# Kernel tuning notes

Measured on AMD Instinct MI355X. Metric: run time of the kernel, lower is better.

## Reference

```python
import jax, jax.numpy as jnp
import numpy as np

B, S, D = 4, 1024, 1024
H = 16
DK = D // H  # 64
F = 4096
EPS = 1e-6


def layer_norm(x, gamma, beta):
    mu = jnp.mean(x, axis=-1, keepdims=True)
    var = jnp.mean(jnp.square(x - mu), axis=-1, keepdims=True)
    return (x - mu) * jax.lax.rsqrt(var + EPS) * gamma + beta


def setup_inputs() -> dict:
    key = jax.random.key(0)
    ks = jax.random.split(key, 16)
    sd = 0.02
    return {
        "x": jax.random.normal(ks[0], (B, S, D), dtype=jnp.float32),
        "Wq": jax.random.normal(ks[1], (H, D, DK), dtype=jnp.float32) * sd,
        "bq": jnp.zeros((H, DK), dtype=jnp.float32),
        "Wk": jax.random.normal(ks[2], (H, D, DK), dtype=jnp.float32) * sd,
        "bk": jnp.zeros((H, DK), dtype=jnp.float32),
        "Wv": jax.random.normal(ks[3], (H, D, DK), dtype=jnp.float32) * sd,
        "bv": jnp.zeros((H, DK), dtype=jnp.float32),
        "Wo": jax.random.normal(ks[4], (D, D), dtype=jnp.float32) * sd,
        "bo": jnp.zeros((D,), dtype=jnp.float32),
        "W1": jax.random.normal(ks[5], (D, F), dtype=jnp.float32) * sd,
        "b1": jnp.zeros((F,), dtype=jnp.float32),
        "W2": jax.random.normal(ks[6], (F, D), dtype=jnp.float32) * sd,
        "b2": jnp.zeros((D,), dtype=jnp.float32),
        "g1": jnp.ones((D,), dtype=jnp.float32),
        "be1": jnp.zeros((D,), dtype=jnp.float32),
        "g2": jnp.ones((D,), dtype=jnp.float32),
        "be2": jnp.zeros((D,), dtype=jnp.float32),
    }


def reference(x, Wq, bq, Wk, bk, Wv, bv, Wo, bo, W1, b1, W2, b2, g1, be1, g2, be2):
    # Per-head Dense projections, expressed as one batched einsum.
    # q/k/v: [B, H, S, DK]
    q = jnp.einsum('bsd,hdk->bhsk', x, Wq) + bq[:, None, :]
    k = jnp.einsum('bsd,hdk->bhsk', x, Wk) + bk[:, None, :]
    v = jnp.einsum('bsd,hdk->bhsk', x, Wv) + bv[:, None, :]
    scale = 1.0 / jnp.sqrt(jnp.float32(DK))
    scores = jnp.einsum('bhqk,bhsk->bhqs', q, k) * scale  # [B,H,S,S]
    attn = jax.nn.softmax(scores, axis=-1)
    ctx = jnp.einsum('bhqs,bhsk->bhqk', attn, v)  # [B,H,S,DK]
    # concat heads along last dim -> [B,S,D]
    ctx = jnp.transpose(ctx, (0, 2, 1, 3)).reshape(B, S, D)
    mh = ctx @ Wo + bo
    # dropout is identity at inference
    h1 = layer_norm(mh + x, g1, be1)
    ffn = jax.nn.relu(h1 @ W1 + b1) @ W2 + b2
    out = layer_norm(h1 + ffn, g2, be2)
    return out
```

## Files before the change

### kernel.cpp

```cpp
#include <hip/hip_runtime.h>
#include <hip/hip_bf16.h>
#include <stdint.h>


typedef __bf16 bf16x8 __attribute__((ext_vector_type(8)));
typedef __bf16 bf16x4 __attribute__((ext_vector_type(4)));
typedef float f32x4 __attribute__((ext_vector_type(4)));

__device__ __forceinline__ f32x4 mfma16(bf16x8 a, bf16x8 b, f32x4 c) {
  return __builtin_amdgcn_mfma_f32_16x16x32_bf16(a, b, c, 0, 0, 0);
}

__device__ __forceinline__ void gload_lds16(const void* g, void* l) {
  typedef const unsigned int __attribute__((address_space(1)))* GP;
  typedef unsigned int __attribute__((address_space(3)))* LP;
  __builtin_amdgcn_global_load_lds((GP)(uintptr_t)g,
                                   (LP)(unsigned int)(uintptr_t)l, 16, 0, 0);
}

template <int EPI>
__global__ __launch_bounds__(512, 2) void gemm256(
    const __bf16* __restrict__ A, const __bf16* __restrict__ BT,
    const float* __restrict__ bias, __bf16* __restrict__ Cb,
    int M, int N, int K)
{
  __shared__ __attribute__((aligned(16))) __bf16 lds[2][2][2][8192];
  const int tid = threadIdx.x;
  const int lane = tid & 63;
  const int w = tid >> 6;
  const int l15 = lane & 15, lhi = lane >> 4;

  const int nbx = gridDim.x;
  const int nwg = nbx * gridDim.y;
  const int wid = blockIdx.y * nbx + blockIdx.x;
  const int sw = (wid & 7) * (nwg >> 3) + (wid >> 3);
  const int n0 = (sw % nbx) * 256;
  const int m0 = (sw / nbx) * 256;

  const int mat = w >> 2, halfI = (w >> 1) & 1, sub = w & 1;
  const __bf16* srcM = mat ? BT : A;
  const long rowG = (long)((mat ? n0 : m0) + halfI * 128 + sub * 64 + (lane >> 3));
  const __bf16* gsrc =
      srcM + rowG * K + (((lane & 7) ^ ((lane >> 3) & 7)) << 3);
  const int ldst = sub * 4096 + lane * 8;

  const int owr = w >> 2, owc = w & 3;

  const f32x4 fz = {0.f, 0.f, 0.f, 0.f};
  f32x4 acc[8][4];
#pragma unroll
  for (int i = 0; i < 8; i++)
#pragma unroll
    for (int j = 0; j < 4; j++) acc[i][j] = fz;

  const int KT = K >> 6;
  const int swz = (l15 & 7);

#pragma unroll
  for (int i = 0; i < 8; i++)
    gload_lds16(gsrc + (long)i * 8 * K, &lds[0][mat][halfI][ldst + i * 512]);

  for (int kt = 0; kt < KT; ++kt) {
    const int buf = kt & 1;
    if (kt + 1 < KT) {
#pragma unroll
      for (int i = 0; i < 8; i++)
        gload_lds16(gsrc + (long)(kt + 1) * 64 + (long)i * 8 * K,
                    &lds[buf ^ 1][mat][halfI][ldst + i * 512]);
      asm volatile("s_waitcnt vmcnt(8)" ::: "memory");
    } else {
      asm volatile("s_waitcnt vmcnt(0)" ::: "memory");
    }
    __builtin_amdgcn_s_barrier();
    __builtin_amdgcn_sched_barrier(0);

    const __bf16* Abase = &lds[buf][0][owr][0];
    const __bf16* Bbase = &lds[buf][1][owc >> 1][0];
    const int brow0 = (owc & 1) * 64;

    bf16x8 bfr[4][2];
#pragma unroll
    for (int nf = 0; nf < 4; nf++)
#pragma unroll
      for (int kk = 0; kk < 2; kk++) {
        const int row = brow0 + nf * 16 + l15;
        bfr[nf][kk] =
            *(const bf16x8*)&Bbase[row * 64 + ((((kk << 2) | lhi) ^ swz) << 3)];
      }

#pragma unroll
    for (int q = 0; q < 4; q++) {
      bf16x8 af[2][2];
#pragma unroll
      for (int m2 = 0; m2 < 2; m2++)
#pragma unroll
        for (int kk = 0; kk < 2; kk++) {
          const int row = (q * 2 + m2) * 16 + l15;
          af[m2][kk] =
              *(const bf16x8*)&Abase[row * 64 + ((((kk << 2) | lhi) ^ swz) << 3)];
        }
      __builtin_amdgcn_s_barrier();
      __builtin_amdgcn_s_setprio(1);
#pragma unroll
      for (int m2 = 0; m2 < 2; m2++)
#pragma unroll
        for (int nf = 0; nf < 4; nf++)
#pragma unroll
          for (int kk = 0; kk < 2; kk++)
            acc[q * 2 + m2][nf] =
                mfma16(af[m2][kk], bfr[nf][kk], acc[q * 2 + m2][nf]);
      __builtin_amdgcn_s_setprio(0);
      __builtin_amdgcn_s_barrier();
    }
  }

  if (EPI == 0) {
#pragma unroll
    for (int mi = 0; mi < 8; mi++) {
      const int mB = m0 + owr * 128 + mi * 16 + lhi * 4;
#pragma unroll
      for (int nf = 0; nf < 4; nf++) {
        const int n = n0 + owc * 64 + nf * 16 + l15;
        const int proj = n >> 10, hh = (n >> 6) & 15, dk = n & 63;
        const float bs = bias[n];
#pragma unroll
        for (int rr = 0; rr < 4; rr++) {
          const int m = mB + rr;
          const int b = m >> 10, sidx = m & 1023;
          Cb[(long)proj * 4194304 +
             ((long)(b * 16 + hh) * 1024 + sidx) * 64 + dk] =
              (__bf16)(acc[mi][nf][rr] + bs);
        }
      }
    }
  } else {
#pragma unroll
    for (int mi = 0; mi < 8; mi++) {
      const int mB = m0 + owr * 128 + mi * 16 + lhi * 4;
#pragma unroll
      for (int nf = 0; nf < 4; nf++) {
        const int n = n0 + owc * 64 + nf * 16 + l15;
        const float bs = bias[n];
#pragma unroll
        for (int rr = 0; rr < 4; rr++) {
          float v = acc[mi][nf][rr] + bs;
          v = v > 0.f ? v : 0.f;
          Cb[(long)(mB + rr) * N + n] = (__bf16)v;
        }
      }
    }
  }
}

__global__ __launch_bounds__(256, 2) void gemm_bt_split(
    const __bf16* __restrict__ A, const __bf16* __restrict__ BT,
    const float* __restrict__ bias, float* __restrict__ Cf0,
    float* __restrict__ Cf1, int M, int N, int ld, int Kh)
{
  __shared__ __attribute__((aligned(16))) __bf16 As[128 * 32];
  __shared__ __attribute__((aligned(16))) __bf16 Bs[128 * 32];
  const int tid = threadIdx.x;
  const int lane = tid & 63;
  const int w = tid >> 6;
  const int wr = w >> 1, wc = w & 1;
  const int l15 = lane & 15, lhi = lane >> 4;
  const int m0 = blockIdx.y * 128, n0 = blockIdx.x * 128;
  const int z = blockIdx.z;

  const f32x4 fz = {0.f, 0.f, 0.f, 0.f};
  f32x4 acc[4][4];
#pragma unroll
  for (int i = 0; i < 4; i++)
#pragma unroll
    for (int j = 0; j < 4; j++) acc[i][j] = fz;

  const int arow = tid >> 2;
  const int acol = (tid & 3) * 8;
  const __bf16* Ag = A + (long)(m0 + arow) * ld + z * Kh + acol;
  const __bf16* Bg = BT + (long)(n0 + arow) * ld + z * Kh + acol;
  __bf16* Al = &As[tid * 8];
  __bf16* Bl = &Bs[tid * 8];

  for (int k0 = 0; k0 < Kh; k0 += 32) {
    gload_lds16(Ag + k0, Al);
    gload_lds16(Ag + k0 + 64 * (long)ld, Al + 2048);
    gload_lds16(Bg + k0, Bl);
    gload_lds16(Bg + k0 + 64 * (long)ld, Bl + 2048);
    __syncthreads();
    bf16x8 a[4], b[4];
#pragma unroll
    for (int i = 0; i < 4; i++) {
      a[i] = *(const bf16x8*)&As[(wr * 64 + i * 16 + l15) * 32 + lhi * 8];
      b[i] = *(const bf16x8*)&Bs[(wc * 64 + i * 16 + l15) * 32 + lhi * 8];
    }
#pragma unroll
    for (int i = 0; i < 4; i++)
#pragma unroll
      for (int j = 0; j < 4; j++) acc[i][j] = mfma16(a[i], b[j], acc[i][j]);
    __syncthreads();
  }

  float* Cf = z ? Cf1 : Cf0;
#pragma unroll
  for (int i = 0; i < 4; i++) {
    const int mB = m0 + wr * 64 + i * 16 + lhi * 4;
#pragma unroll
    for (int j = 0; j < 4; j++) {
      const int n = n0 + wc * 64 + j * 16 + l15;
      const float bs = z ? 0.f : bias[n];
#pragma unroll
      for (int r = 0; r < 4; r++)
        Cf[(long)(mB + r) * N + n] = acc[i][j][r] + bs;
    }
  }
}

__global__ __launch_bounds__(256) void vtrans_kernel(
    const __bf16* __restrict__ in, __bf16* __restrict__ out)
{
  __shared__ __bf16 t[64][66];
  const int bh = blockIdx.y, s0 = blockIdx.x * 64;
  const int tx = threadIdx.x & 63, ty = threadIdx.x >> 6;
  const __bf16* ip = in + (long)bh * 65536 + (long)s0 * 64;
  __bf16* op = out + (long)bh * 65536;
#pragma unroll
  for (int i = 0; i < 64; i += 4) t[ty + i][tx] = ip[(ty + i) * 64 + tx];
  __syncthreads();
#pragma unroll
  for (int i = 0; i < 64; i += 4)
    op[(long)(ty + i) * 1024 + s0 + tx] = t[tx][ty + i];
}

__global__ __launch_bounds__(256, 2) void attn_kernel(
    const __bf16* __restrict__ qg_, const __bf16* __restrict__ kg_,
    const __bf16* __restrict__ vtg_, __bf16* __restrict__ ctx)
{
  __shared__ __attribute__((aligned(16))) __bf16 Kb[2][64 * 64];
  __shared__ __attribute__((aligned(16))) __bf16 Vb[2][64 * 64];
  __shared__ __attribute__((aligned(16))) __bf16 Ps[4][16 * 64];
  const int tid = threadIdx.x, lane = tid & 63, w = tid >> 6;
  const int l15 = lane & 15, lhi = lane >> 4;
  const int bh = blockIdx.y;
  const int b = bh >> 4, h = bh & 15;
  const int q0 = blockIdx.x * 64 + w * 16;

  const __bf16* qg = qg_ + ((long)bh * 1024 + q0) * 64;
  const __bf16* kg = kg_ + (long)bh * 65536;
  const __bf16* vtg = vtg_ + (long)bh * 65536;

  bf16x8 qa[2];
  qa[0] = *(const bf16x8*)&qg[l15 * 64 + lhi * 8];
  qa[1] = *(const bf16x8*)&qg[l15 * 64 + 32 + lhi * 8];

  const int srow0 = tid >> 3;
  const int srow1 = srow0 + 32;
  const int sw0 = (tid & 7) ^ (srow0 & 7);
  const int sw1 = (tid & 7) ^ (srow1 & 7);
  const __bf16* kst0 = kg + srow0 * 64 + sw0 * 8;
  const __bf16* kst1 = kg + srow1 * 64 + sw1 * 8;
  const __bf16* vst0 = vtg + srow0 * 1024 + sw0 * 8;
  const __bf16* vst1 = vtg + srow1 * 1024 + sw1 * 8;

  const f32x4 fz = {0.f, 0.f, 0.f, 0.f};
  float mrun[4], lrun[4];
  f32x4 o[4];
#pragma unroll
  for (int r = 0; r < 4; r++) { mrun[r] = -1e30f; lrun[r] = 0.f; }
#pragma unroll
  for (int n = 0; n < 4; n++) o[n] = fz;

  const int e = l15 & 7;
  const int c0 = (lhi ^ e) * 8;
  const int c1 = ((4 | lhi) ^ e) * 8;

  {
    __bf16* kb = &Kb[0][tid * 8];
    __bf16* vb = &Vb[0][tid * 8];
    gload_lds16(kst0, kb);
    gload_lds16(kst1, kb + 2048);
    gload_lds16(vst0, vb);
    gload_lds16(vst1, vb + 2048);
  }

  int cur = 0;
  for (int t = 0; t < 16; ++t) {
    __syncthreads();
    if (t + 1 < 16) {
      __bf16* kb = &Kb[cur ^ 1][tid * 8];
      __bf16* vb = &Vb[cur ^ 1][tid * 8];
      gload_lds16(kst0 + (t + 1) * 4096, kb);
      gload_lds16(kst1 + (t + 1) * 4096, kb + 2048);
      gload_lds16(vst0 + (t + 1) * 64, vb);
      gload_lds16(vst1 + (t + 1) * 64, vb + 2048);
    }

    f32x4 s[4];
#pragma unroll
    for (int n = 0; n < 4; n++) s[n] = fz;
    __builtin_amdgcn_s_setprio(1);
#pragma unroll
    for (int n = 0; n < 4; n++) {
      const int row = (n * 16 + l15) * 64;
      bf16x8 kb0 = *(const bf16x8*)&Kb[cur][row + c0];
      bf16x8 kb1 = *(const bf16x8*)&Kb[cur][row + c1];
      s[n] = mfma16(qa[0], kb0, s[n]);
      s[n] = mfma16(qa[1], kb1, s[n]);
    }
    __builtin_amdgcn_s_setprio(0);

    float alpha[4];
    float p[4][4];
#pragma unroll
    for (int r = 0; r < 4; r++) {
      float mx = -1e30f;
#pragma unroll
      for (int n = 0; n < 4; n++) {
        s[n][r] *= 0.125f;
        mx = fmaxf(mx, s[n][r]);
      }
#pragma unroll
      for (int off = 8; off; off >>= 1) mx = fmaxf(mx, __shfl_xor(mx, off));
      const float mnew = fmaxf(mrun[r], mx);
      alpha[r] = __expf(mrun[r] - mnew);
      float ps = 0.f;
#pragma unroll
      for (int n = 0; n < 4; n++) {
        const float pv = __expf(s[n][r] - mnew);
        p[n][r] = pv;
        ps += pv;
      }
#pragma unroll
      for (int off = 8; off; off >>= 1) ps += __shfl_xor(ps, off);
      mrun[r] = mnew;
      lrun[r] = lrun[r] * alpha[r] + ps;
    }
#pragma unroll
    for (int n = 0; n < 4; n++)
#pragma unroll
      for (int r = 0; r < 4; r++) o[n][r] *= alpha[r];

#pragma unroll
    for (int n = 0; n < 4; n++) {
      const int ch = n * 2 + (l15 >> 3);
#pragma unroll
      for (int r = 0; r < 4; r++) {
        const int row = lhi * 4 + r;
        Ps[w][row * 64 + (ch ^ (row & 7)) * 8 + e] = (__bf16)p[n][r];
      }
    }
    asm volatile("s_waitcnt lgkmcnt(0)" ::: "memory");

    __builtin_amdgcn_s_setprio(1);
#pragma unroll
    for (int kk = 0; kk < 2; kk++) {
      bf16x8 pa = *(const bf16x8*)&Ps[w][l15 * 64 + (kk ? c1 : c0)];
#pragma unroll
      for (int n = 0; n < 4; n++) {
        bf16x8 vb =
            *(const bf16x8*)&Vb[cur][(n * 16 + l15) * 64 + (kk ? c1 : c0)];
        o[n] = mfma16(pa, vb, o[n]);
      }
    }
    __builtin_amdgcn_s_setprio(0);
    cur ^= 1;
  }

  const long crow = (long)b * 1024 + q0;
#pragma unroll
  for (int n = 0; n < 4; n++)
#pragma unroll
    for (int r = 0; r < 4; r++) {
      const float val = o[n][r] / lrun[r];
      ctx[(crow + lhi * 4 + r) * 1024 + h * 64 + n * 16 + l15] = (__bf16)val;
    }
}

template <int CB, int OB>
__global__ __launch_bounds__(256) void ln_fuse3(
    const float* __restrict__ a, const float* __restrict__ b,
    const void* __restrict__ c_, const float* __restrict__ gamma,
    const float* __restrict__ beta, float* __restrict__ outf,
    __bf16* __restrict__ outb)
{
  const int row = blockIdx.x;
  const int tid = threadIdx.x;
  const float4 va = ((const float4*)(a + (long)row * 1024))[tid];
  const float4 vb = ((const float4*)(b + (long)row * 1024))[tid];
  float c0, c1, c2, c3;
  if (CB) {
    const bf16x4 cv =
        *(const bf16x4*)((const __bf16*)c_ + (long)row * 1024 + tid * 4);
    c0 = (float)cv[0]; c1 = (float)cv[1]; c2 = (float)cv[2]; c3 = (float)cv[3];
  } else {
    const float4 vc = ((const float4*)((const float*)c_ + (long)row * 1024))[tid];
    c0 = vc.x; c1 = vc.y; c2 = vc.z; c3 = vc.w;
  }
  const float x0 = va.x + vb.x + c0, x1 = va.y + vb.y + c1,
              x2 = va.z + vb.z + c2, x3 = va.w + vb.w + c3;
  float sum = x0 + x1 + x2 + x3;
  float sq = x0 * x0 + x1 * x1 + x2 * x2 + x3 * x3;
#pragma unroll
  for (int off = 32; off; off >>= 1) {
    sum += __shfl_down(sum, off);
    sq += __shfl_down(sq, off);
  }
  __shared__ float red[8];
  const int w = tid >> 6;
  if ((tid & 63) == 0) { red[w] = sum; red[4 + w] = sq; }
  __syncthreads();
  sum = red[0] + red[1] + red[2] + red[3];
  sq = red[4] + red[5] + red[6] + red[7];
  const float mean = sum * (1.f / 1024.f);
  const float var = sq * (1.f / 1024.f) - mean * mean;
  const float inv = rsqrtf(var + 1e-6f);
  const float4 g = ((const float4*)gamma)[tid];
  const float4 be = ((const float4*)beta)[tid];
  const float y0 = (x0 - mean) * inv * g.x + be.x;
  const float y1 = (x1 - mean) * inv * g.y + be.y;
  const float y2 = (x2 - mean) * inv * g.z + be.z;
  const float y3 = (x3 - mean) * inv * g.w + be.w;
  if (OB) {
    __bf16* ob = outb + (long)row * 1024 + tid * 4;
    ob[0] = (__bf16)y0; ob[1] = (__bf16)y1;
    ob[2] = (__bf16)y2; ob[3] = (__bf16)y3;
  } else {
    float4 o4; o4.x = y0; o4.y = y1; o4.z = y2; o4.w = y3;
    ((float4*)(outf + (long)row * 1024))[tid] = o4;
  }
}

__global__ __launch_bounds__(256) void cast_bf16_kernel(
    const float* __restrict__ in, __bf16* __restrict__ out, int n4)
{
  const int i = blockIdx.x * 256 + threadIdx.x;
  if (i < n4) {
    const float4 v = ((const float4*)in)[i];
    __bf16* o = out + (long)i * 4;
    o[0] = (__bf16)v.x; o[1] = (__bf16)v.y;
    o[2] = (__bf16)v.z; o[3] = (__bf16)v.w;
  }
}

__global__ __launch_bounds__(256) void pack_bias_kernel(
    const float* __restrict__ bq, const float* __restrict__ bk,
    const float* __restrict__ bv, float* __restrict__ out)
{
  const int i = blockIdx.x * 256 + threadIdx.x;
  if (i < 3072) {
    const float* src = i < 1024 ? bq : (i < 2048 ? bk : bv);
    out[i] = src[i & 1023];
  }
}

__global__ __launch_bounds__(256) void transpose_cast_kernel(
    const float* __restrict__ in, __bf16* __restrict__ out, int R, int C,
    long ibs, long obs)
{
  __shared__ float t[32][33];
  const float* ip = in + (long)blockIdx.z * ibs;
  __bf16* op = out + (long)blockIdx.z * obs;
  const int c0 = blockIdx.x * 32, r0 = blockIdx.y * 32;
  const int tx = threadIdx.x & 31, ty = threadIdx.x >> 5;
#pragma unroll
  for (int i = 0; i < 32; i += 8)
    t[ty + i][tx] = ip[(long)(r0 + ty + i) * C + (c0 + tx)];
  __syncthreads();
#pragma unroll
  for (int i = 0; i < 32; i += 8)
    op[(long)(c0 + ty + i) * R + (r0 + tx)] = (__bf16)t[tx][ty + i];
}

extern "C" void kernel_launch(void* const* d_in, const int* in_sizes, int n_in,
                              void* d_out, int out_size, void* d_ws,
                              size_t ws_size, hipStream_t stream)
{
  const float* x   = (const float*)d_in[0];
  const float* Wq  = (const float*)d_in[1];
  const float* bq  = (const float*)d_in[2];
  const float* Wk  = (const float*)d_in[3];
  const float* bk  = (const float*)d_in[4];
  const float* Wv  = (const float*)d_in[5];
  const float* bv  = (const float*)d_in[6];
  const float* Wo  = (const float*)d_in[7];
  const float* bo  = (const float*)d_in[8];
  const float* W1  = (const float*)d_in[9];
  const float* b1  = (const float*)d_in[10];
  const float* W2  = (const float*)d_in[11];
  const float* b2  = (const float*)d_in[12];
  const float* g1  = (const float*)d_in[13];
  const float* be1 = (const float*)d_in[14];
  const float* g2  = (const float*)d_in[15];
  const float* be2 = (const float*)d_in[16];
  float* out = (float*)d_out;

  char* ws = (char*)d_ws;
  __bf16* wqkvT = (__bf16*)(ws);
  __bf16* woT   = (__bf16*)(ws + 6291456);
  __bf16* w1T   = (__bf16*)(ws + 8388608);
  __bf16* w2T   = (__bf16*)(ws + 16777216);
  float*  bqkv  = (float*)(ws + 25165824);
  __bf16* xbf   = (__bf16*)(ws + 25178112);
  __bf16* ctxb  = xbf;
  __bf16* qkv   = (__bf16*)(ws + 33566720);
  float*  mh_p1 = (float*)(ws + 33566720);
  __bf16* h1b   = (__bf16*)(ws + 50343936);
  __bf16* f1b   = (__bf16*)(ws + 58732544);
  float*  f2_p1 = (float*)(ws + 25178112);
  __bf16* vt    = (__bf16*)d_out;
  float*  mh_p0 = out;
  float*  f2_p0 = out;

  cast_bf16_kernel<<<4096, 256, 0, stream>>>(x, xbf, 1048576);
  pack_bias_kernel<<<12, 256, 0, stream>>>(bq, bk, bv, bqkv);
  transpose_cast_kernel<<<dim3(2, 32, 16), 256, 0, stream>>>(
      Wq, wqkvT, 1024, 64, 65536, 65536);
  transpose_cast_kernel<<<dim3(2, 32, 16), 256, 0, stream>>>(
      Wk, wqkvT + 1048576, 1024, 64, 65536, 65536);
  transpose_cast_kernel<<<dim3(2, 32, 16), 256, 0, stream>>>(
      Wv, wqkvT + 2097152, 1024, 64, 65536, 65536);
  transpose_cast_kernel<<<dim3(32, 32, 1), 256, 0, stream>>>(
      Wo, woT, 1024, 1024, 0, 0);
  transpose_cast_kernel<<<dim3(128, 32, 1), 256, 0, stream>>>(
      W1, w1T, 1024, 4096, 0, 0);
  transpose_cast_kernel<<<dim3(32, 128, 1), 256, 0, stream>>>(
      W2, w2T, 4096, 1024, 0, 0);

  gemm256<0><<<dim3(12, 16), 512, 0, stream>>>(
      xbf, wqkvT, bqkv, qkv, 4096, 3072, 1024);

  vtrans_kernel<<<dim3(16, 64), 256, 0, stream>>>(qkv + 8388608, vt);

  attn_kernel<<<dim3(16, 64), 256, 0, stream>>>(
      qkv, qkv + 4194304, vt, ctxb);

  gemm_bt_split<<<dim3(8, 32, 2), 256, 0, stream>>>(
      ctxb, woT, bo, mh_p0, mh_p1, 4096, 1024, 1024, 512);

  ln_fuse3<0, 1><<<4096, 256, 0, stream>>>(
      mh_p0, mh_p1, x, g1, be1, nullptr, h1b);

  gemm256<1><<<dim3(16, 16), 512, 0, stream>>>(
      h1b, w1T, b1, f1b, 4096, 4096, 1024);

  gemm_bt_split<<<dim3(8, 32, 2), 256, 0, stream>>>(
      f1b, w2T, b2, f2_p0, f2_p1, 4096, 1024, 4096, 2048);

  ln_fuse3<1, 0><<<4096, 256, 0, stream>>>(
      f2_p0, f2_p1, h1b, g2, be2, out, nullptr);
}
```

Baseline: 374.9 us.

## Rewrite split-K GEMM with 128x256 tiles, double-buffered swizzled LDS and workgroup remap

```diff
diff --git a/kernel.cpp b/kernel.cpp
--- a/kernel.cpp
+++ b/kernel.cpp
@@ -152,20 +152,37 @@
   }
 }
 
-__global__ __launch_bounds__(256, 2) void gemm_bt_split(
+__global__ __launch_bounds__(512, 2) void gemm_ksplit(
     const __bf16* __restrict__ A, const __bf16* __restrict__ BT,
     const float* __restrict__ bias, float* __restrict__ Cf0,
     float* __restrict__ Cf1, int M, int N, int ld, int Kh)
 {
-  __shared__ __attribute__((aligned(16))) __bf16 As[128 * 32];
-  __shared__ __attribute__((aligned(16))) __bf16 Bs[128 * 32];
+  __shared__ __attribute__((aligned(16))) __bf16 As[2][8192];
+  __shared__ __attribute__((aligned(16))) __bf16 Bs[2][16384];
   const int tid = threadIdx.x;
   const int lane = tid & 63;
   const int w = tid >> 6;
-  const int wr = w >> 1, wc = w & 1;
   const int l15 = lane & 15, lhi = lane >> 4;
-  const int m0 = blockIdx.y * 128, n0 = blockIdx.x * 128;
-  const int z = blockIdx.z;
+
+  const int nbx = gridDim.x;
+  const int nby = gridDim.y;
+  const int nxy = nbx * nby;
+  const int nwg = nxy * 2;
+  const int wid = (blockIdx.z * nby + blockIdx.y) * nbx + blockIdx.x;
+  const int sw = (wid & 7) * (nwg >> 3) + (wid >> 3);
+  const int z = sw / nxy;
+  const int rem = sw % nxy;
+  const int m0 = (rem / nbx) * 128;
+  const int n0 = (rem % nbx) * 256;
+  const long zoff = (long)z * Kh;
+
+  const int trow = tid >> 3;
+  const int sswz = ((tid & 7) ^ (trow & 7)) << 3;
+  const __bf16* gA = A + (long)(m0 + trow) * ld + zoff + sswz;
+  const __bf16* gB = BT + (long)(n0 + trow) * ld + zoff + sswz;
+  const int ldst = tid * 8;
+
+  const int owr = w >> 2, owc = w & 3;
 
   const f32x4 fz = {0.f, 0.f, 0.f, 0.f};
   f32x4 acc[4][4];
@@ -174,43 +191,81 @@
 #pragma unroll
     for (int j = 0; j < 4; j++) acc[i][j] = fz;
 
-  const int arow = tid >> 2;
-  const int acol = (tid & 3) * 8;
-  const __bf16* Ag = A + (long)(m0 + arow) * ld + z * Kh + acol;
-  const __bf16* Bg = BT + (long)(n0 + arow) * ld + z * Kh + acol;
-  __bf16* Al = &As[tid * 8];
-  __bf16* Bl = &Bs[tid * 8];
-
-  for (int k0 = 0; k0 < Kh; k0 += 32) {
-    gload_lds16(Ag + k0, Al);
-    gload_lds16(Ag + k0 + 64 * (long)ld, Al + 2048);
-    gload_lds16(Bg + k0, Bl);
-    gload_lds16(Bg + k0 + 64 * (long)ld, Bl + 2048);
-    __syncthreads();
-    bf16x8 a[4], b[4];
-#pragma unroll
-    for (int i = 0; i < 4; i++) {
-      a[i] = *(const bf16x8*)&As[(wr * 64 + i * 16 + l15) * 32 + lhi * 8];
-      b[i] = *(const bf16x8*)&Bs[(wc * 64 + i * 16 + l15) * 32 + lhi * 8];
-    }
-#pragma unroll
-    for (int i = 0; i < 4; i++)
-#pragma unroll
-      for (int j = 0; j < 4; j++) acc[i][j] = mfma16(a[i], b[j], acc[i][j]);
-    __syncthreads();
+  const int KT = Kh >> 6;
+  const int swz = (l15 & 7);
+
+  {
+    gload_lds16(gA, &As[0][ldst]);
+    gload_lds16(gA + 64 * (long)ld, &As[0][ldst + 4096]);
+    gload_lds16(gB, &Bs[0][ldst]);
+    gload_lds16(gB + 64 * (long)ld, &Bs[0][ldst + 4096]);
+    gload_lds16(gB + 128 * (long)ld, &Bs[0][ldst + 8192]);
+    gload_lds16(gB + 192 * (long)ld, &Bs[0][ldst + 12288]);
+  }
+
+  for (int kt = 0; kt < KT; ++kt) {
+    const int buf = kt & 1;
+    if (kt + 1 < KT) {
+      const __bf16* a0 = gA + (kt + 1) * 64;
+      const __bf16* b0 = gB + (kt + 1) * 64;
+      gload_lds16(a0, &As[buf ^ 1][ldst]);
+      gload_lds16(a0 + 64 * (long)ld, &As[buf ^ 1][ldst + 4096]);
+      gload_lds16(b0, &Bs[buf ^ 1][ldst]);
+      gload_lds16(b0 + 64 * (long)ld, &Bs[buf ^ 1][ldst + 4096]);
+      gload_lds16(b0 + 128 * (long)ld, &Bs[buf ^ 1][ldst + 8192]);
+      gload_lds16(b0 + 192 * (long)ld, &Bs[buf ^ 1][ldst + 12288]);
+      asm volatile("s_waitcnt vmcnt(6)" ::: "memory");
+    } else {
+      asm volatile("s_waitcnt vmcnt(0)" ::: "memory");
+    }
+    __builtin_amdgcn_s_barrier();
+    __builtin_amdgcn_sched_barrier(0);
+
+    const __bf16* Abase = &As[buf][owr * 4096];
+    const __bf16* Bbase = &Bs[buf][owc * 4096];
+
+    bf16x8 bfr[4][2];
+#pragma unroll
+    for (int nf = 0; nf < 4; nf++)
+#pragma unroll
+      for (int kk = 0; kk < 2; kk++) {
+        const int row = nf * 16 + l15;
+        bfr[nf][kk] =
+            *(const bf16x8*)&Bbase[row * 64 + ((((kk << 2) | lhi) ^ swz) << 3)];
+      }
+
+#pragma unroll
+    for (int q = 0; q < 4; q++) {
+      bf16x8 af[2];
+#pragma unroll
+      for (int kk = 0; kk < 2; kk++) {
+        const int row = q * 16 + l15;
+        af[kk] =
+            *(const bf16x8*)&Abase[row * 64 + ((((kk << 2) | lhi) ^ swz) << 3)];
+      }
+      __builtin_amdgcn_s_barrier();
+      __builtin_amdgcn_s_setprio(1);
+#pragma unroll
+      for (int nf = 0; nf < 4; nf++)
+#pragma unroll
+        for (int kk = 0; kk < 2; kk++)
+          acc[q][nf] = mfma16(af[kk], bfr[nf][kk], acc[q][nf]);
+      __builtin_amdgcn_s_setprio(0);
+      __builtin_amdgcn_s_barrier();
+    }
   }
 
   float* Cf = z ? Cf1 : Cf0;
 #pragma unroll
-  for (int i = 0; i < 4; i++) {
-    const int mB = m0 + wr * 64 + i * 16 + lhi * 4;
-#pragma unroll
-    for (int j = 0; j < 4; j++) {
-      const int n = n0 + wc * 64 + j * 16 + l15;
+  for (int mi = 0; mi < 4; mi++) {
+    const int mB = m0 + owr * 64 + mi * 16 + lhi * 4;
+#pragma unroll
+    for (int nf = 0; nf < 4; nf++) {
+      const int n = n0 + owc * 64 + nf * 16 + l15;
       const float bs = z ? 0.f : bias[n];
 #pragma unroll
-      for (int r = 0; r < 4; r++)
-        Cf[(long)(mB + r) * N + n] = acc[i][j][r] + bs;
+      for (int rr = 0; rr < 4; rr++)
+        Cf[(long)(mB + rr) * N + n] = acc[mi][nf][rr] + bs;
     }
   }
 }
@@ -533,7 +588,7 @@
   attn_kernel<<<dim3(16, 64), 256, 0, stream>>>(
       qkv, qkv + 4194304, vt, ctxb);
 
-  gemm_bt_split<<<dim3(8, 32, 2), 256, 0, stream>>>(
+  gemm_ksplit<<<dim3(4, 32, 2), 512, 0, stream>>>(
       ctxb, woT, bo, mh_p0, mh_p1, 4096, 1024, 1024, 512);
 
   ln_fuse3<0, 1><<<4096, 256, 0, stream>>>(
@@ -542,7 +597,7 @@
   gemm256<1><<<dim3(16, 16), 512, 0, stream>>>(
       h1b, w1T, b1, f1b, 4096, 4096, 1024);
 
-  gemm_bt_split<<<dim3(8, 32, 2), 256, 0, stream>>>(
+  gemm_ksplit<<<dim3(4, 32, 2), 512, 0, stream>>>(
       f1b, w2T, b2, f2_p0, f2_p1, 4096, 1024, 4096, 2048);
 
   ln_fuse3<1, 0><<<4096, 256, 0, stream>>>(
```

Result: faster. 358.2 us (-4.5%).
